# Performance work log

Hardware: AMD Instinct MI355X
Metric: run time of the kernel (lower is better)

Reference implementation:

```python
import jax, jax.numpy as jnp
import numpy as np
import math

B, S, U, H = 8, 1024, 1024, 16
DK = U // H  # 64


def setup_inputs() -> dict:
    key = jax.random.key(0)
    ks = jax.random.split(key, 12)
    query = jax.random.normal(ks[0], (B, S, U), jnp.float32)
    key_t = jax.random.normal(ks[1], (B, S, U), jnp.float32)  # unused by module (bug preserved)
    value = jax.random.normal(ks[2], (B, S, U), jnp.float32)  # unused by module (bug preserved)
    # causal multiplicative 0/1 mask [B,S,S]
    mask = jnp.broadcast_to(jnp.tril(jnp.ones((S, S), jnp.float32)), (B, S, S))
    bh = math.sqrt(1.0 / DK)   # init bound for per-head projections (out_features=d_k)
    bo = math.sqrt(1.0 / U)    # init bound for output projection (out_features=n_units)
    u = lambda k, shape, b: jax.random.uniform(k, shape, jnp.float32, -b, b)
    # per-head weights stacked: [H, U, DK] (already input->output layout)
    Wq = u(ks[3], (H, U, DK), bh); bq = u(ks[4], (H, DK), bh)
    Wk = u(ks[5], (H, U, DK), bh); bk = u(ks[6], (H, DK), bh)
    Wv = u(ks[7], (H, U, DK), bh); bv = u(ks[8], (H, DK), bh)
    Wo = u(ks[9], (U, U), bo);     bo_ = u(ks[10], (U,), bo)
    return dict(query=query, key=key_t, value=value, mask=mask,
                Wq=Wq, bq=bq, Wk=Wk, bk=bk, Wv=Wv, bv=bv, Wo=Wo, bo=bo_)


def reference(query, key, value, mask, Wq, bq, Wk, bk, Wv, bv, Wo, bo):
    # NOTE: faithful to source — q, k, v are ALL projected from `query`.
    q = jnp.einsum('bsu,hud->bhsd', query, Wq) + bq[:, None, :]
    k = jnp.einsum('bsu,hud->bhsd', query, Wk) + bk[:, None, :]
    v = jnp.einsum('bsu,hud->bhsd', query, Wv) + bv[:, None, :]
    scores = jnp.einsum('bhqd,bhkd->bhqk', q, k) / math.sqrt(DK)
    s = mask[:, None, :, :]  # broadcast over heads
    x = scores * s - 1e9 * (1.0 - s)  # multiplicative mask baked into softmax input
    attn = jax.nn.softmax(x, axis=-1)
    out = jnp.einsum('bhqk,bhkd->bhqd', attn, v)
    # concat heads along feature dim (head 0 first, matching torch.cat order)
    out = out.transpose(0, 2, 1, 3).reshape(B, S, U)
    return out @ Wo + bo
```

## Files before the change

### kernel.cpp

```cpp
#include <hip/hip_runtime.h>
#include <hip/hip_bf16.h>

#define B_ 8
#define S_ 1024
#define U_ 1024
#define H_ 16
#define DK_ 64

typedef __attribute__((ext_vector_type(8))) short short8;
typedef __attribute__((ext_vector_type(4))) float f32x4;
typedef __attribute__((ext_vector_type(16))) float f32x16;

__device__ inline ushort f2b(float x) {
  union { float f; unsigned u; } v; v.f = x;
  unsigned r = (v.u + 0x7FFFu + ((v.u >> 16) & 1u)) >> 16;
  return (ushort)r;
}
__device__ inline unsigned pk2(float lo, float hi) {
  return (unsigned)f2b(lo) | ((unsigned)f2b(hi) << 16);
}

__device__ inline void gld16(const ushort* g, ushort* l) {
  __builtin_amdgcn_global_load_lds((__attribute__((address_space(1))) void*)(g),
                                   (__attribute__((address_space(3))) void*)(l),
                                   16, 0, 0);
}

__global__ __launch_bounds__(256) void pack_x_kern(const float* __restrict__ X,
                                                   ushort* __restrict__ Xb) {
  int idx = blockIdx.x * 256 + threadIdx.x;
  const float4* src = (const float4*)X + (size_t)idx * 2;
  float4 a = src[0], b = src[1];
  ushort r[8];
  r[0]=f2b(a.x); r[1]=f2b(a.y); r[2]=f2b(a.z); r[3]=f2b(a.w);
  r[4]=f2b(b.x); r[5]=f2b(b.y); r[6]=f2b(b.z); r[7]=f2b(b.w);
  *(uint4*)(Xb + (size_t)idx*8) = *(uint4*)r;
}

__global__ __launch_bounds__(256) void pack_w_kern(
    const float* __restrict__ Wq, const float* __restrict__ Wk, const float* __restrict__ Wv,
    const float* __restrict__ bq, const float* __restrict__ bk, const float* __restrict__ bv,
    const float* __restrict__ Wo,
    ushort* __restrict__ Wqkv, float* __restrict__ Bqkv, ushort* __restrict__ Wob)
{
  __shared__ ushort tile[64*65];
  const int t = threadIdx.x;
  const int bid = blockIdx.x;
  if (bid < 768) {
    int p = bid >> 8, rem = bid & 255;
    int h = rem >> 4, kc = rem & 15, k0 = kc*64;
    const float* Wsrc = (p==0) ? Wq : ((p==1) ? Wk : Wv);
    #pragma unroll
    for (int i = 0; i < 16; ++i) {
      int e = t + i*256;
      int r = e >> 6, d = e & 63;
      tile[d*65 + r] = f2b(Wsrc[h*65536 + (k0+r)*64 + d]);
    }
    __syncthreads();
    #pragma unroll
    for (int i = 0; i < 16; ++i) {
      int e = t + i*256;
      int d = e >> 6, r = e & 63;
      Wqkv[(size_t)(p*1024 + h*64 + d)*1024 + k0 + r] = tile[d*65 + r];
    }
    if (kc == 0 && t < 64) {
      const float* bsrc = (p==0) ? bq : ((p==1) ? bk : bv);
      Bqkv[p*1024 + h*64 + t] = bsrc[h*64 + t];
    }
  } else {
    int b2 = bid - 768;
    int nc = b2 >> 4, kc = b2 & 15;
    int n0 = nc*64, k0 = kc*64;
    #pragma unroll
    for (int i = 0; i < 16; ++i) {
      int e = t + i*256;
      int r = e >> 6, d = e & 63;
      tile[d*65 + r] = f2b(Wo[(size_t)(k0+r)*1024 + n0 + d]);
    }
    __syncthreads();
    #pragma unroll
    for (int i = 0; i < 16; ++i) {
      int e = t + i*256;
      int d = e >> 6, r = e & 63;
      Wob[(size_t)(n0+d)*1024 + k0 + r] = tile[d*65 + r];
    }
  }
}

template<int MODE>
__global__ __launch_bounds__(256, 4) void gemm128_kern(
    const ushort* __restrict__ A,
    const ushort* __restrict__ Bw,
    const float* __restrict__ bias,
    ushort* __restrict__ Qb, ushort* __restrict__ Kb, ushort* __restrict__ Vtb,
    float* __restrict__ outF)
{
  __shared__ __align__(16) ushort As[2][4096];
  __shared__ __align__(16) ushort Bs[2][4096];

  const int t = threadIdx.x;
  const int l = t & 63, w = t >> 6;
  const int wr = w >> 1, wc = w & 1;
  const int li = l & 15, c4 = l >> 4;

  int m0, n0;
  if (MODE==0) {
    int swz = (blockIdx.x & 7) * 192 + (blockIdx.x >> 3);
    int ms = swz / 192, rem = swz % 192;
    m0 = (ms*8 + (rem & 7)) * 128;  n0 = (rem >> 3) * 128;
  } else {
    int swz = (blockIdx.x & 7) * 64 + (blockIdx.x >> 3);
    int ms = swz / 64, rem = swz % 64;
    m0 = (ms*8 + (rem & 7)) * 128;  n0 = (rem >> 3) * 128;
  }

  f32x4 acc[4][4];
  #pragma unroll
  for (int i=0;i<4;i++)
    #pragma unroll
    for (int j=0;j<4;j++) acc[i][j] = (f32x4)0.0f;

  auto SA = [&](int buf, int kk) {
    #pragma unroll
    for (int p2=0;p2<2;++p2) {
      int n = p2*256 + t;
      int row = n >> 2, jj = (n & 3) ^ ((row >> 1) & 3);
      gld16(&A[(size_t)(m0 + row)*1024 + kk + jj*8], &As[buf][n*8]);
    }
  };
  auto SB = [&](int buf, int kk) {
    #pragma unroll
    for (int p2=0;p2<2;++p2) {
      int n = p2*256 + t;
      int row = n >> 2, jj = (n & 3) ^ ((row >> 1) & 3);
      gld16(&Bw[(size_t)(n0 + row)*1024 + kk + jj*8], &Bs[buf][n*8]);
    }
  };

  SA(0, 0);  SB(0, 0);
  SA(1, 32); SB(1, 32);

  for (int kt = 0; kt < 32; ++kt) {
    const int cur = kt & 1;
    asm volatile("s_waitcnt vmcnt(4)" ::: "memory");
    __builtin_amdgcn_s_barrier();
    __builtin_amdgcn_sched_barrier(0);

    short8 af[4], bf[4];
    #pragma unroll
    for (int i=0;i<4;i++) {
      int rA = wr*64 + i*16 + li;
      int rB = wc*64 + i*16 + li;
      af[i] = *(const short8*)&As[cur][rA*32 + ((c4 ^ ((rA>>1)&3))*8)];
      bf[i] = *(const short8*)&Bs[cur][rB*32 + ((c4 ^ ((rB>>1)&3))*8)];
    }
    __builtin_amdgcn_s_setprio(1);
    #pragma unroll
    for (int i=0;i<4;i++)
      #pragma unroll
      for (int j=0;j<4;j++)
        acc[i][j] = __builtin_amdgcn_mfma_f32_16x16x32_bf16(af[i], bf[j], acc[i][j], 0,0,0);
    __builtin_amdgcn_s_setprio(0);

    __builtin_amdgcn_s_barrier();
    __builtin_amdgcn_sched_barrier(0);
    const int kk2 = ((kt + 2) & 31) * 32;
    SA(cur, kk2); SB(cur, kk2);
  }

  #pragma unroll
  for (int i=0;i<4;i++) {
    int rbase = m0 + wr*64 + i*16 + c4*4;
    #pragma unroll
    for (int j=0;j<4;j++) {
      int col = n0 + wc*64 + j*16 + li;
      float bv = bias[col];
      if (MODE == 0) {
        int p = col >> 10, h = (col >> 6) & 15, d = col & 63;
        int b = rbase >> 10, s = rbase & 1023;
        if (p == 2) {
          ushort pk4[4];
          #pragma unroll
          for (int r=0;r<4;r++) pk4[r] = f2b(acc[i][j][r] + bv);
          *(uint2*)&Vtb[((size_t)((b*16+h)*64 + d))*1024 + s] = *(uint2*)pk4;
        } else {
          ushort* dst = (p==0) ? Qb : Kb;
          float sc = (p==0) ? 0.18033688011112042f : 1.0f;
          #pragma unroll
          for (int r=0;r<4;r++)
            dst[(((size_t)(b*16 + h))*1024 + s + r)*64 + d] = f2b((acc[i][j][r] + bv) * sc);
        }
      } else {
        #pragma unroll
        for (int r=0;r<4;r++)
          outF[(size_t)(rbase+r)*1024 + col] = acc[i][j][r] + bv;
      }
    }
  }
}

__global__ __launch_bounds__(256, 2) void attn_kern(
    const ushort* __restrict__ Qb, const ushort* __restrict__ Kb,
    const ushort* __restrict__ Vt, ushort* __restrict__ Ob)
{
  __shared__ __align__(16) ushort Pb[4][32*40];
  __shared__ __align__(16) ushort OT[4][32*72];
  const int t = threadIdx.x, l = t & 63, w = t >> 6;
  const int bid = blockIdx.x;
  const int x = bid & 7, i0 = bid >> 3;
  const int bh = x*16 + (i0 >> 2);
  const int p  = (i0 & 3)*4 + w;
  const int qta = p, qtb = 31 - p;

  const int col = l & 31, hi = l >> 5;
  const ushort* Qp = Qb + (size_t)bh*65536;
  const ushort* Kp = Kb + (size_t)bh*65536;
  const ushort* Vp = Vt + (size_t)bh*65536;

  short8 qfa[4], qfb[4];
  #pragma unroll
  for (int m=0;m<4;m++) {
    qfa[m] = *(const short8*)&Qp[(size_t)(qta*32+col)*64 + m*16 + hi*8];
    qfb[m] = *(const short8*)&Qp[(size_t)(qtb*32+col)*64 + m*16 + hi*8];
  }

  f32x16 aA0 = (f32x16)0.0f, aA1 = (f32x16)0.0f;
  f32x16 aB0 = (f32x16)0.0f, aB1 = (f32x16)0.0f;
  float mA = -1e30f, lA = 0.0f, mB = -1e30f, lB = 0.0f;
  ushort* Pw = &Pb[w][0];

  auto PROC = [&](f32x16& s, bool diag, float& mR, float& lS,
                  f32x16& o0, f32x16& o1, const short8* vf0, const short8* vf1) {
    if (diag) {
      #pragma unroll
      for (int r=0;r<16;r++) {
        int kvl = (r&3) + ((r>>2)<<3) + 4*hi;
        s[r] = (kvl > col) ? -1e9f : s[r];
      }
    }
    float mx = s[0];
    #pragma unroll
    for (int r=1;r<16;r++) mx = fmaxf(mx, s[r]);
    mx = fmaxf(mx, __shfl_xor(mx, 32));
    if (__any(mx - mR > 8.0f)) {
      float mN = fmaxf(mR, mx);
      float corr = __builtin_amdgcn_exp2f(mR - mN);
      mR = mN; lS *= corr;
      #pragma unroll
      for (int r=0;r<16;r++) { o0[r] *= corr; o1[r] *= corr; }
    }
    float pr[16], rs = 0.0f;
    #pragma unroll
    for (int r=0;r<16;r++) { pr[r] = __builtin_amdgcn_exp2f(s[r] - mR); rs += pr[r]; }
    rs += __shfl_xor(rs, 32);
    lS += rs;
    #pragma unroll
    for (int r2=0;r2<8;r2++) {
      int r = 2*r2;
      int kv = (r&3) + ((r>>2)<<3) + 4*hi;
      *(unsigned*)&Pw[col*40 + kv] = pk2(pr[r], pr[r+1]);
    }
    short8 pb0 = *(const short8*)&Pw[col*40 + hi*8];
    short8 pb1 = *(const short8*)&Pw[col*40 + 16 + hi*8];
    o0 = __builtin_amdgcn_mfma_f32_32x32x16_bf16(vf0[0], pb0, o0, 0,0,0);
    o0 = __builtin_amdgcn_mfma_f32_32x32x16_bf16(vf0[1], pb1, o0, 0,0,0);
    o1 = __builtin_amdgcn_mfma_f32_32x32x16_bf16(vf1[0], pb0, o1, 0,0,0);
    o1 = __builtin_amdgcn_mfma_f32_32x32x16_bf16(vf1[1], pb1, o1, 0,0,0);
  };

  for (int kt = 0; kt <= qtb; ++kt) {
    short8 kf[4], vf0[2], vf1[2];
    #pragma unroll
    for (int m=0;m<4;m++)
      kf[m] = *(const short8*)&Kp[(size_t)(kt*32+col)*64 + m*16 + hi*8];
    #pragma unroll
    for (int m=0;m<2;m++) {
      vf0[m] = *(const short8*)&Vp[(size_t)col*1024      + kt*32 + m*16 + hi*8];
      vf1[m] = *(const short8*)&Vp[(size_t)(32+col)*1024 + kt*32 + m*16 + hi*8];
    }

    f32x16 sB = (f32x16)0.0f;
    #pragma unroll
    for (int m=0;m<4;m++)
      sB = __builtin_amdgcn_mfma_f32_32x32x16_bf16(kf[m], qfb[m], sB, 0, 0, 0);
    PROC(sB, kt == qtb, mB, lB, aB0, aB1, vf0, vf1);

    if (kt <= qta) {
      f32x16 sA = (f32x16)0.0f;
      #pragma unroll
      for (int m=0;m<4;m++)
        sA = __builtin_amdgcn_mfma_f32_32x32x16_bf16(kf[m], qfa[m], sA, 0, 0, 0);
      PROC(sA, kt == qta, mA, lA, aA0, aA1, vf0, vf1);
    }
  }

  const int b = bh >> 4, h = bh & 15;
  auto EPI = [&](int qt, float lS, const f32x16& o0, const f32x16& o1) {
    float inv = 1.0f / lS;
    ushort* o = &OT[w][0];
    #pragma unroll
    for (int r2=0;r2<8;r2++) {
      int r = 2*r2;
      int dv = (r&3) + ((r>>2)<<3) + 4*hi;
      *(unsigned*)&o[col*72 + dv]      = pk2(o0[r]*inv, o0[r+1]*inv);
      *(unsigned*)&o[col*72 + 32 + dv] = pk2(o1[r]*inv, o1[r+1]*inv);
    }
    #pragma unroll
    for (int it=0; it<4; ++it) {
      int q = it*8 + (l>>3), c8 = (l&7)*8;
      uint4 v = *(const uint4*)&o[q*72 + c8];
      int qg = qt*32 + q;
      *(uint4*)&Ob[(size_t)(b*1024+qg)*1024 + h*64 + c8] = v;
    }
  };
  EPI(qta, lA, aA0, aA1);
  EPI(qtb, lB, aB0, aB1);
}

extern "C" void kernel_launch(void* const* d_in, const int* in_sizes, int n_in,
                              void* d_out, int out_size, void* d_ws, size_t ws_size,
                              hipStream_t stream) {
  const float* query = (const float*)d_in[0];
  const float* Wq = (const float*)d_in[4];
  const float* bq = (const float*)d_in[5];
  const float* Wk = (const float*)d_in[6];
  const float* bk = (const float*)d_in[7];
  const float* Wv = (const float*)d_in[8];
  const float* bv = (const float*)d_in[9];
  const float* Wo = (const float*)d_in[10];
  const float* bo = (const float*)d_in[11];

  char* wsb = (char*)d_ws;
  ushort* Xb   = (ushort*)(wsb);
  ushort* Wqkv = (ushort*)(wsb + 16777216);
  float*  Bqkv = (float*) (wsb + 23068672);
  ushort* Wob  = (ushort*)(wsb + 23080960);
  ushort* Qb   = (ushort*)(wsb + 25178112);
  ushort* Kb   = (ushort*)(wsb + 41955328);
  ushort* Vtb  = (ushort*)(wsb + 58732544);
  ushort* Ob   = (ushort*)(wsb + 75509760);

  hipLaunchKernelGGL(pack_x_kern, dim3(4096), dim3(256), 0, stream, query, Xb);
  hipLaunchKernelGGL(pack_w_kern, dim3(1024), dim3(256), 0, stream,
                     Wq, Wk, Wv, bq, bk, bv, Wo, Wqkv, Bqkv, Wob);
  hipLaunchKernelGGL(gemm128_kern<0>, dim3(1536), dim3(256), 0, stream,
                     Xb, Wqkv, Bqkv, Qb, Kb, Vtb, (float*)nullptr);
  hipLaunchKernelGGL(attn_kern, dim3(512), dim3(256), 0, stream, Qb, Kb, Vtb, Ob);
  hipLaunchKernelGGL(gemm128_kern<1>, dim3(512), dim3(256), 0, stream,
                     Ob, Wob, bo, (ushort*)nullptr, (ushort*)nullptr, (ushort*)nullptr,
                     (float*)d_out);
}
```

Baseline: 167.8 us.

## Deepen GEMM K-tile to 64 and prefetch next K/V tile in attention

The projection GEMM kernel now stages 64-wide K slices per iteration with an 8-way XOR swizzle. That halves the barrier and wait count per K-loop, at the cost of doubled LDS and a lower launch-bounds occupancy hint. The attention loop now loads the next K/V fragments into registers before computing the current tile. It also issues both query-tile score MFMAs before the softmax processing, so global loads and MFMA latency overlap with the exp work. The risks are higher register pressure and reduced occupancy.

```diff
diff --git a/kernel.cpp b/kernel.cpp
--- a/kernel.cpp
+++ b/kernel.cpp
@@ -88,15 +88,15 @@
 }
 
 template<int MODE>
-__global__ __launch_bounds__(256, 4) void gemm128_kern(
+__global__ __launch_bounds__(256, 2) void gemm128_kern(
     const ushort* __restrict__ A,
     const ushort* __restrict__ Bw,
     const float* __restrict__ bias,
     ushort* __restrict__ Qb, ushort* __restrict__ Kb, ushort* __restrict__ Vtb,
     float* __restrict__ outF)
 {
-  __shared__ __align__(16) ushort As[2][4096];
-  __shared__ __align__(16) ushort Bs[2][4096];
+  __shared__ __align__(16) ushort As[2][8192];
+  __shared__ __align__(16) ushort Bs[2][8192];
 
   const int t = threadIdx.x;
   const int l = t & 63, w = t >> 6;
@@ -122,50 +122,57 @@
 
   auto SA = [&](int buf, int kk) {
     #pragma unroll
-    for (int p2=0;p2<2;++p2) {
-      int n = p2*256 + t;
-      int row = n >> 2, jj = (n & 3) ^ ((row >> 1) & 3);
+    for (int p=0;p<4;++p) {
+      int n = p*256 + t;
+      int row = n >> 3, jj = (n & 7) ^ (row & 7);
       gld16(&A[(size_t)(m0 + row)*1024 + kk + jj*8], &As[buf][n*8]);
     }
   };
   auto SB = [&](int buf, int kk) {
     #pragma unroll
-    for (int p2=0;p2<2;++p2) {
-      int n = p2*256 + t;
-      int row = n >> 2, jj = (n & 3) ^ ((row >> 1) & 3);
+    for (int p=0;p<4;++p) {
+      int n = p*256 + t;
+      int row = n >> 3, jj = (n & 7) ^ (row & 7);
       gld16(&Bw[(size_t)(n0 + row)*1024 + kk + jj*8], &Bs[buf][n*8]);
     }
   };
 
   SA(0, 0);  SB(0, 0);
-  SA(1, 32); SB(1, 32);
-
-  for (int kt = 0; kt < 32; ++kt) {
+  SA(1, 64); SB(1, 64);
+  asm volatile("s_waitcnt vmcnt(8)" ::: "memory");
+  __builtin_amdgcn_s_barrier();
+  __builtin_amdgcn_sched_barrier(0);
+
+  for (int kt = 0; kt < 16; ++kt) {
     const int cur = kt & 1;
-    asm volatile("s_waitcnt vmcnt(4)" ::: "memory");
-    __builtin_amdgcn_s_barrier();
-    __builtin_amdgcn_sched_barrier(0);
-
-    short8 af[4], bf[4];
+    short8 af[4][2], bf[4][2];
     #pragma unroll
     for (int i=0;i<4;i++) {
       int rA = wr*64 + i*16 + li;
       int rB = wc*64 + i*16 + li;
-      af[i] = *(const short8*)&As[cur][rA*32 + ((c4 ^ ((rA>>1)&3))*8)];
-      bf[i] = *(const short8*)&Bs[cur][rB*32 + ((c4 ^ ((rB>>1)&3))*8)];
+      #pragma unroll
+      for (int ks=0;ks<2;ks++) {
+        af[i][ks] = *(const short8*)&As[cur][rA*64 + (((ks*4+c4)^(li&7))*8)];
+        bf[i][ks] = *(const short8*)&Bs[cur][rB*64 + (((ks*4+c4)^(li&7))*8)];
+      }
     }
     __builtin_amdgcn_s_setprio(1);
     #pragma unroll
     for (int i=0;i<4;i++)
       #pragma unroll
       for (int j=0;j<4;j++)
-        acc[i][j] = __builtin_amdgcn_mfma_f32_16x16x32_bf16(af[i], bf[j], acc[i][j], 0,0,0);
+        #pragma unroll
+        for (int ks=0;ks<2;ks++)
+          acc[i][j] = __builtin_amdgcn_mfma_f32_16x16x32_bf16(af[i][ks], bf[j][ks], acc[i][j], 0,0,0);
     __builtin_amdgcn_s_setprio(0);
 
     __builtin_amdgcn_s_barrier();
     __builtin_amdgcn_sched_barrier(0);
-    const int kk2 = ((kt + 2) & 31) * 32;
+    const int kk2 = ((kt + 2) & 15) * 64;
     SA(cur, kk2); SB(cur, kk2);
+    asm volatile("s_waitcnt vmcnt(8)" ::: "memory");
+    __builtin_amdgcn_s_barrier();
+    __builtin_amdgcn_sched_barrier(0);
   }
 
   #pragma unroll
@@ -268,30 +275,43 @@
     o1 = __builtin_amdgcn_mfma_f32_32x32x16_bf16(vf1[1], pb1, o1, 0,0,0);
   };
 
+  auto LOADKV = [&](int kt, short8* kf_, short8* v0_, short8* v1_) {
+    #pragma unroll
+    for (int m=0;m<4;m++)
+      kf_[m] = *(const short8*)&Kp[(size_t)(kt*32+col)*64 + m*16 + hi*8];
+    #pragma unroll
+    for (int m=0;m<2;m++) {
+      v0_[m] = *(const short8*)&Vp[(size_t)col*1024      + kt*32 + m*16 + hi*8];
+      v1_[m] = *(const short8*)&Vp[(size_t)(32+col)*1024 + kt*32 + m*16 + hi*8];
+    }
+  };
+
+  short8 kf[4], vf0[2], vf1[2];
+  LOADKV(0, kf, vf0, vf1);
+
   for (int kt = 0; kt <= qtb; ++kt) {
-    short8 kf[4], vf0[2], vf1[2];
-    #pragma unroll
-    for (int m=0;m<4;m++)
-      kf[m] = *(const short8*)&Kp[(size_t)(kt*32+col)*64 + m*16 + hi*8];
-    #pragma unroll
-    for (int m=0;m<2;m++) {
-      vf0[m] = *(const short8*)&Vp[(size_t)col*1024      + kt*32 + m*16 + hi*8];
-      vf1[m] = *(const short8*)&Vp[(size_t)(32+col)*1024 + kt*32 + m*16 + hi*8];
-    }
-
-    f32x16 sB = (f32x16)0.0f;
+    short8 kf2[4], v02[2], v12[2];
+    const int ktn = (kt + 1 <= qtb) ? kt + 1 : qtb;
+    LOADKV(ktn, kf2, v02, v12);
+
+    const bool doA = (kt <= qta);
+    f32x16 sB = (f32x16)0.0f, sA = (f32x16)0.0f;
     #pragma unroll
     for (int m=0;m<4;m++)
       sB = __builtin_amdgcn_mfma_f32_32x32x16_bf16(kf[m], qfb[m], sB, 0, 0, 0);
-    PROC(sB, kt == qtb, mB, lB, aB0, aB1, vf0, vf1);
-
-    if (kt <= qta) {
-      f32x16 sA = (f32x16)0.0f;
+    if (doA) {
       #pragma unroll
       for (int m=0;m<4;m++)
         sA = __builtin_amdgcn_mfma_f32_32x32x16_bf16(kf[m], qfa[m], sA, 0, 0, 0);
-      PROC(sA, kt == qta, mA, lA, aA0, aA1, vf0, vf1);
-    }
+    }
+
+    PROC(sB, kt == qtb, mB, lB, aB0, aB1, vf0, vf1);
+    if (doA) PROC(sA, kt == qta, mA, lA, aA0, aA1, vf0, vf1);
+
+    #pragma unroll
+    for (int m=0;m<4;m++) kf[m] = kf2[m];
+    #pragma unroll
+    for (int m=0;m<2;m++) { vf0[m] = v02[m]; vf1[m] = v12[m]; }
   }
 
   const int b = bh >> 4, h = bh & 15;
```

New measurement: 164.6 us. About the same (-1.9%).
